# Kernel optimization log

Measured on AMD Instinct MI355X. Metric: run time of the kernel, lower is better.

## Reference

```python
import jax, jax.numpy as jnp
import numpy as np

N_NODES = 100000
N_EDGES = 3200000
IN_DIM = 128
HID = 128
K = 20  # n_gaussians


def gcn_conv(x, src, dst, W, b, n_nodes):
    """PyG GCNConv: add self-loops, symmetric normalization, linear transform.
    out = D^{-1/2} (A + I) D^{-1/2} (x @ W) + b, where D is degree of A+I.
    """
    h = x @ W  # [N, out_dim]
    # degree on A + I (self-loop contributes 1 to every node)
    deg = jax.ops.segment_sum(jnp.ones_like(dst, dtype=h.dtype), dst,
                              num_segments=n_nodes) + 1.0
    dis = jax.lax.rsqrt(deg)  # deg >= 1, safe
    norm = dis[src] * dis[dst]  # [E]
    # gather -> scale -> scatter-add (edges), plus self-loop term dis_i^2 * h_i
    agg = jax.ops.segment_sum(h[src] * norm[:, None], dst,
                              num_segments=n_nodes)
    agg = agg + h * (dis * dis)[:, None]
    return agg + b


def setup_inputs() -> dict:
    key = jax.random.key(0)
    ks = jax.random.split(key, 12)
    x = jax.random.normal(ks[0], (N_NODES, IN_DIM), dtype=jnp.float32)
    edge_index = jax.random.randint(ks[1], (2, N_EDGES), 0, N_NODES, dtype=jnp.int32)
    s = 1.0 / np.sqrt(HID)
    W1 = jax.random.uniform(ks[2], (IN_DIM, HID), jnp.float32, -s, s)
    b1 = jnp.zeros((HID,), jnp.float32)
    W2 = jax.random.uniform(ks[3], (HID, HID), jnp.float32, -s, s)
    b2 = jnp.zeros((HID,), jnp.float32)
    pi_W = jax.random.uniform(ks[4], (HID, K), jnp.float32, -s, s)
    pi_b = jnp.zeros((K,), jnp.float32)
    mu_W = jax.random.uniform(ks[5], (HID, K), jnp.float32, -s, s)
    mu_b = jnp.zeros((K,), jnp.float32)
    ls_W = jax.random.uniform(ks[6], (HID, K), jnp.float32, -s, s)
    ls_b = jnp.zeros((K,), jnp.float32)
    return {"x": x, "edge_index": edge_index, "W1": W1, "b1": b1,
            "W2": W2, "b2": b2, "pi_W": pi_W, "pi_b": pi_b,
            "mu_W": mu_W, "mu_b": mu_b, "ls_W": ls_W, "ls_b": ls_b}


def reference(x, edge_index, W1, b1, W2, b2, pi_W, pi_b, mu_W, mu_b, ls_W, ls_b):
    src, dst = edge_index[0], edge_index[1]
    n = x.shape[0]
    h = jax.nn.relu(gcn_conv(x, src, dst, W1, b1, n))
    h = jax.nn.relu(gcn_conv(h, src, dst, W2, b2, n))
    pi = jax.nn.softmax(h @ pi_W + pi_b, axis=1)
    mu = h @ mu_W + mu_b
    log_sigma = h @ ls_W + ls_b
    return (pi, mu, log_sigma)
```

## Files before the change

kernel.cpp:

```cpp
#include <hip/hip_runtime.h>
#include <hip/hip_fp16.h>
#include <cstdint>
#include <cstddef>

#define IN_DIM 128
#define HID    128
#define NG     20
#define T      4096
#define MAXB   400

typedef _Float16 half8 __attribute__((ext_vector_type(8)));
typedef _Float16 half4 __attribute__((ext_vector_type(4)));
typedef float    f32x4 __attribute__((ext_vector_type(4)));

__global__ void zero_ints(int* __restrict__ a, int n) {
  int i = blockIdx.x * blockDim.x + threadIdx.x;
  if (i < n) a[i] = 0;
}

__global__ __launch_bounds__(512) void binsort1(const int* __restrict__ src,
    const int* __restrict__ dst, int* __restrict__ tmp, int* __restrict__ bofs,
    int* __restrict__ bintot, int NBC, int E) {
  __shared__ int lhist[MAXB];
  __shared__ int lscan[512];
  __shared__ int lcur[MAXB];
  __shared__ int sbuf[T];
  int tid = threadIdx.x;
  int tile0 = blockIdx.x * T;
  int m = E - tile0; if (m > T) m = T;

  for (int i = tid; i < NBC; i += 512) lhist[i] = 0;
  __syncthreads();

  int dreg[8];
#pragma unroll
  for (int j = 0; j < 8; ++j) {
    int idx = j * 512 + tid;
    dreg[j] = -1;
    if (idx < m) {
      int d = dst[tile0 + idx];
      dreg[j] = d;
      atomicAdd(&lhist[d >> 8], 1);
    }
  }
  __syncthreads();

  int v = (tid < NBC) ? lhist[tid] : 0;
  lscan[tid] = v;
  __syncthreads();
  for (int o = 1; o < 512; o <<= 1) {
    int t = (tid >= o) ? lscan[tid - o] : 0;
    __syncthreads();
    lscan[tid] += t;
    __syncthreads();
  }
  if (tid < NBC) lcur[tid] = lscan[tid] - v;
  __syncthreads();

  int ST = NBC + 1;
  for (int i = tid; i < NBC; i += 512) bofs[(size_t)blockIdx.x * ST + i] = lcur[i];
  if (tid == 0) bofs[(size_t)blockIdx.x * ST + NBC] = m;
  for (int i = tid; i < NBC; i += 512)
    if (lhist[i]) atomicAdd(&bintot[i], lhist[i]);
  __syncthreads();

#pragma unroll
  for (int j = 0; j < 8; ++j) {
    int idx = j * 512 + tid;
    if (idx < m) {
      int d = dreg[j];
      int s = src[tile0 + idx];
      int slot = atomicAdd(&lcur[d >> 8], 1);
      sbuf[slot] = ((d & 255) << 17) | s;
    }
  }
  __syncthreads();

  int nv = m >> 2;
  int4* out4 = (int4*)(tmp + tile0);
  const int4* sb4 = (const int4*)sbuf;
  for (int i = tid; i < nv; i += 512) out4[i] = sb4[i];
  for (int i = (nv << 2) + tid; i < m; i += 512) tmp[tile0 + i] = sbuf[i];
}

__global__ __launch_bounds__(512) void binscan(const int* __restrict__ bintot,
                                               int* __restrict__ binbase, int NBC) {
  __shared__ int s[512];
  int tid = threadIdx.x;
  int v = (tid < NBC) ? bintot[tid] : 0;
  s[tid] = v;
  __syncthreads();
  for (int o = 1; o < 512; o <<= 1) {
    int t = (tid >= o) ? s[tid - o] : 0;
    __syncthreads();
    s[tid] += t;
    __syncthreads();
  }
  if (tid < NBC) binbase[tid] = s[tid] - v;
}

__global__ __launch_bounds__(1024) void binsort2(const int* __restrict__ tmp,
    const int* __restrict__ bofs, const int* __restrict__ binbase,
    int* __restrict__ csrc, int* __restrict__ cnt, float* __restrict__ dis,
    int* __restrict__ offs, int NBC, int nblk, int N) {
  __shared__ int lcnt[256];
  __shared__ int lsc[256];
  __shared__ int lcur2[256];
  int b = blockIdx.x;
  int tid = threadIdx.x;
  if (tid < 256) lcnt[tid] = 0;
  __syncthreads();
  int ST = NBC + 1;
  for (int r = tid; r < nblk; r += 1024) {
    int s = bofs[(size_t)r * ST + b];
    int e2 = bofs[(size_t)r * ST + b + 1];
    int base = r * T;
    for (int k = s; k < e2; ++k)
      atomicAdd(&lcnt[tmp[base + k] >> 17], 1);
  }
  __syncthreads();
  if (tid < 256) lsc[tid] = lcnt[tid];
  __syncthreads();
  for (int o = 1; o < 256; o <<= 1) {
    int t = 0;
    if (tid < 256 && tid >= o) t = lsc[tid - o];
    __syncthreads();
    if (tid < 256) lsc[tid] += t;
    __syncthreads();
  }
  int gbase = binbase[b];
  if (tid < 256) {
    int excl = lsc[tid] - lcnt[tid];
    lcur2[tid] = gbase + excl;
    int node = (b << 8) + tid;
    if (node < N) {
      cnt[node] = lcnt[tid];
      dis[node] = rsqrtf((float)lcnt[tid] + 1.0f);
      offs[node] = gbase + excl;
    }
  }
  __syncthreads();
  for (int r = tid; r < nblk; r += 1024) {
    int s = bofs[(size_t)r * ST + b];
    int e2 = bofs[(size_t)r * ST + b + 1];
    int base = r * T;
    for (int k = s; k < e2; ++k) {
      int rec = tmp[base + k];
      int pos = atomicAdd(&lcur2[rec >> 17], 1);
      csrc[pos] = rec & 0x1FFFF;
    }
  }
}

__global__ __launch_bounds__(256) void gemm128_mfma(const float* __restrict__ A,
                                                    const float* __restrict__ B,
                                                    __half* __restrict__ C, int M) {
  __shared__ _Float16 sA[128][136];
  const int tid = threadIdx.x;
  const int m0 = blockIdx.x * 128;

#pragma unroll
  for (int q = 0; q < 16; ++q) {
    int idx = q * 256 + tid;
    int r = idx >> 5;
    int cc = (idx & 31) << 2;
    float4 v = make_float4(0.f, 0.f, 0.f, 0.f);
    if (m0 + r < M) v = *(const float4*)(A + (size_t)(m0 + r) * 128 + cc);
    half4 hv;
    hv[0] = (_Float16)v.x; hv[1] = (_Float16)v.y;
    hv[2] = (_Float16)v.z; hv[3] = (_Float16)v.w;
    *(half4*)(&sA[r][cc]) = hv;
  }
  __syncthreads();

  const int wave = tid >> 6, lane = tid & 63;
  const int nbase = wave << 5;
  const int lrow = lane & 15;
  const int khi  = lane >> 4;

  half8 bf[2][4];
#pragma unroll
  for (int nf = 0; nf < 2; ++nf) {
    const float* wcol = B + (nbase + nf * 16 + lrow);
#pragma unroll
    for (int ks = 0; ks < 4; ++ks) {
      half8 hb;
#pragma unroll
      for (int rr = 0; rr < 8; ++rr)
        hb[rr] = (_Float16)wcol[(size_t)(ks * 32 + khi * 8 + rr) * 128];
      bf[nf][ks] = hb;
    }
  }

  f32x4 acc[8][2];
#pragma unroll
  for (int mf = 0; mf < 8; ++mf)
#pragma unroll
    for (int nf = 0; nf < 2; ++nf) acc[mf][nf] = (f32x4){0.f, 0.f, 0.f, 0.f};

#pragma unroll
  for (int mf = 0; mf < 8; ++mf) {
    const _Float16* ar = &sA[mf * 16 + lrow][khi * 8];
    half8 a0 = *(const half8*)(ar);
    half8 a1 = *(const half8*)(ar + 32);
    half8 a2 = *(const half8*)(ar + 64);
    half8 a3 = *(const half8*)(ar + 96);
    acc[mf][0] = __builtin_amdgcn_mfma_f32_16x16x32_f16(a0, bf[0][0], acc[mf][0], 0, 0, 0);
    acc[mf][1] = __builtin_amdgcn_mfma_f32_16x16x32_f16(a0, bf[1][0], acc[mf][1], 0, 0, 0);
    acc[mf][0] = __builtin_amdgcn_mfma_f32_16x16x32_f16(a1, bf[0][1], acc[mf][0], 0, 0, 0);
    acc[mf][1] = __builtin_amdgcn_mfma_f32_16x16x32_f16(a1, bf[1][1], acc[mf][1], 0, 0, 0);
    acc[mf][0] = __builtin_amdgcn_mfma_f32_16x16x32_f16(a2, bf[0][2], acc[mf][0], 0, 0, 0);
    acc[mf][1] = __builtin_amdgcn_mfma_f32_16x16x32_f16(a2, bf[1][2], acc[mf][1], 0, 0, 0);
    acc[mf][0] = __builtin_amdgcn_mfma_f32_16x16x32_f16(a3, bf[0][3], acc[mf][0], 0, 0, 0);
    acc[mf][1] = __builtin_amdgcn_mfma_f32_16x16x32_f16(a3, bf[1][3], acc[mf][1], 0, 0, 0);
  }

#pragma unroll
  for (int mf = 0; mf < 8; ++mf) {
    int r0 = mf * 16 + khi * 4;
#pragma unroll
    for (int nf = 0; nf < 2; ++nf) {
      int ccol = nbase + nf * 16 + lrow;
#pragma unroll
      for (int reg = 0; reg < 4; ++reg) {
        int r = m0 + r0 + reg;
        if (r < M) C[(size_t)r * 128 + ccol] = __float2half(acc[mf][nf][reg]);
      }
    }
  }
}

__global__ __launch_bounds__(256) void agg_kernel(const __half* __restrict__ h,
    const int* __restrict__ csrc,
    const int* __restrict__ offs, const int* __restrict__ cnt,
    const float* __restrict__ dis, const float* __restrict__ bias,
    float* __restrict__ out, int n) {
  int wave = threadIdx.x >> 6;
  int lane = threadIdx.x & 63;
  int i0 = (blockIdx.x * 4 + wave) * 2;
  if (i0 >= n) return;
  int i1 = i0 + 1;
  bool has1 = i1 < n;
  int c = lane * 2;

  int st0 = offs[i0];
  int m0  = cnt[i0];
  float d0 = dis[i0];
  int st1 = 0, m1 = 0;
  float d1 = 0.f;
  if (has1) { st1 = offs[i1]; m1 = cnt[i1]; d1 = dis[i1]; }

  float ax0 = 0.f, ay0 = 0.f, ax1 = 0.f, ay1 = 0.f;
  int mMax = m0 > m1 ? m0 : m1;

  for (int base = 0; base < mMax; base += 64) {
    int mcA = m0 - base; mcA = mcA < 0 ? 0 : (mcA > 64 ? 64 : mcA);
    int mcB = m1 - base; mcB = mcB < 0 ? 0 : (mcB > 64 ? 64 : mcB);
    int mc = mcA > mcB ? mcA : mcB;

    int sA = 0, sB = 0;
    float wA = 0.f, wB = 0.f;
    if (lane < mcA) sA = csrc[st0 + base + lane];
    if (lane < mcB) sB = csrc[st1 + base + lane];
    if (lane < mcA) wA = dis[sA] * d0;
    if (lane < mcB) wB = dis[sB] * d1;

    int j = 0;
    for (; j + 4 <= mc; j += 4) {
      int   a0 = __shfl(sA, j);
      int   a1 = __shfl(sA, j + 1);
      int   a2 = __shfl(sA, j + 2);
      int   a3 = __shfl(sA, j + 3);
      int   b0 = __shfl(sB, j);
      int   b1 = __shfl(sB, j + 1);
      int   b2 = __shfl(sB, j + 2);
      int   b3 = __shfl(sB, j + 3);
      float u0 = __shfl(wA, j);
      float u1 = __shfl(wA, j + 1);
      float u2 = __shfl(wA, j + 2);
      float u3 = __shfl(wA, j + 3);
      float v0 = __shfl(wB, j);
      float v1 = __shfl(wB, j + 1);
      float v2 = __shfl(wB, j + 2);
      float v3 = __shfl(wB, j + 3);
      float2 hA0 = __half22float2(*(const __half2*)(h + ((size_t)a0 << 7) + c));
      float2 hA1 = __half22float2(*(const __half2*)(h + ((size_t)a1 << 7) + c));
      float2 hA2 = __half22float2(*(const __half2*)(h + ((size_t)a2 << 7) + c));
      float2 hA3 = __half22float2(*(const __half2*)(h + ((size_t)a3 << 7) + c));
      float2 hB0 = __half22float2(*(const __half2*)(h + ((size_t)b0 << 7) + c));
      float2 hB1 = __half22float2(*(const __half2*)(h + ((size_t)b1 << 7) + c));
      float2 hB2 = __half22float2(*(const __half2*)(h + ((size_t)b2 << 7) + c));
      float2 hB3 = __half22float2(*(const __half2*)(h + ((size_t)b3 << 7) + c));
      ax0 = fmaf(hA0.x, u0, ax0); ay0 = fmaf(hA0.y, u0, ay0);
      ax0 = fmaf(hA1.x, u1, ax0); ay0 = fmaf(hA1.y, u1, ay0);
      ax0 = fmaf(hA2.x, u2, ax0); ay0 = fmaf(hA2.y, u2, ay0);
      ax0 = fmaf(hA3.x, u3, ax0); ay0 = fmaf(hA3.y, u3, ay0);
      ax1 = fmaf(hB0.x, v0, ax1); ay1 = fmaf(hB0.y, v0, ay1);
      ax1 = fmaf(hB1.x, v1, ax1); ay1 = fmaf(hB1.y, v1, ay1);
      ax1 = fmaf(hB2.x, v2, ax1); ay1 = fmaf(hB2.y, v2, ay1);
      ax1 = fmaf(hB3.x, v3, ax1); ay1 = fmaf(hB3.y, v3, ay1);
    }
    for (; j < mc; ++j) {
      int   a0 = __shfl(sA, j);
      int   b0 = __shfl(sB, j);
      float u0 = __shfl(wA, j);
      float v0 = __shfl(wB, j);
      float2 hA0 = __half22float2(*(const __half2*)(h + ((size_t)a0 << 7) + c));
      float2 hB0 = __half22float2(*(const __half2*)(h + ((size_t)b0 << 7) + c));
      ax0 = fmaf(hA0.x, u0, ax0); ay0 = fmaf(hA0.y, u0, ay0);
      ax1 = fmaf(hB0.x, v0, ax1); ay1 = fmaf(hB0.y, v0, ay1);
    }
  }

  float2 bv = *(const float2*)(bias + c);
  {
    float dd = d0 * d0;
    float2 hs = __half22float2(*(const __half2*)(h + ((size_t)i0 << 7) + c));
    float vx = fmaf(hs.x, dd, ax0) + bv.x;
    float vy = fmaf(hs.y, dd, ay0) + bv.y;
    *(float2*)(out + (size_t)i0 * 128 + c) = make_float2(fmaxf(vx, 0.f), fmaxf(vy, 0.f));
  }
  if (has1) {
    float dd = d1 * d1;
    float2 hs = __half22float2(*(const __half2*)(h + ((size_t)i1 << 7) + c));
    float vx = fmaf(hs.x, dd, ax1) + bv.x;
    float vy = fmaf(hs.y, dd, ay1) + bv.y;
    *(float2*)(out + (size_t)i1 * 128 + c) = make_float2(fmaxf(vx, 0.f), fmaxf(vy, 0.f));
  }
}

__global__ void pack_heads_w(const float* __restrict__ piW, const float* __restrict__ muW,
                             const float* __restrict__ lsW, float* __restrict__ W64) {
  int i = blockIdx.x * 256 + threadIdx.x;
  if (i >= 128 * 64) return;
  int k = i >> 6, j = i & 63;
  float v = 0.f;
  if (j < 20)      v = piW[k * 20 + j];
  else if (j < 40) v = muW[k * 20 + (j - 20)];
  else if (j < 60) v = lsW[k * 20 + (j - 40)];
  W64[i] = v;
}

#define KC 64
__global__ __launch_bounds__(256) void gemm_heads(const float* __restrict__ A,
                                                  const float* __restrict__ B,
                                                  float* __restrict__ C, int M) {
  __shared__ float sA[64][KC + 4];
  __shared__ float sB[KC][68];
  int tid = threadIdx.x;
  int m0 = blockIdx.x * 64;
  int tr = tid >> 4;
  int tc = tid & 15;
  float acc[4][4];
#pragma unroll
  for (int i = 0; i < 4; ++i)
#pragma unroll
    for (int j = 0; j < 4; ++j) acc[i][j] = 0.f;

  for (int k0 = 0; k0 < 128; k0 += KC) {
#pragma unroll
    for (int q = 0; q < 4; ++q) {
      int idx = q * 256 + tid;
      int r = idx >> 4;
      int kk = (idx & 15) << 2;
      float4 v = make_float4(0.f, 0.f, 0.f, 0.f);
      if (m0 + r < M) v = *(const float4*)(A + (size_t)(m0 + r) * 128 + k0 + kk);
      *(float4*)(&sA[r][kk]) = v;
    }
#pragma unroll
    for (int q = 0; q < 4; ++q) {
      int idx = q * 256 + tid;
      int kk = idx >> 4;
      int nn = (idx & 15) << 2;
      *(float4*)(&sB[kk][nn]) = *(const float4*)(B + (size_t)(k0 + kk) * 64 + nn);
    }
    __syncthreads();
#pragma unroll 4
    for (int k = 0; k < KC; k += 4) {
      float4 a0 = *(const float4*)(&sA[tr][k]);
      float4 a1 = *(const float4*)(&sA[tr + 16][k]);
      float4 a2 = *(const float4*)(&sA[tr + 32][k]);
      float4 a3 = *(const float4*)(&sA[tr + 48][k]);
#pragma unroll
      for (int u = 0; u < 4; ++u) {
        float4 b = *(const float4*)(&sB[k + u][tc * 4]);
        float av[4] = {((const float*)&a0)[u], ((const float*)&a1)[u],
                       ((const float*)&a2)[u], ((const float*)&a3)[u]};
#pragma unroll
        for (int i = 0; i < 4; ++i) {
          acc[i][0] = fmaf(av[i], b.x, acc[i][0]);
          acc[i][1] = fmaf(av[i], b.y, acc[i][1]);
          acc[i][2] = fmaf(av[i], b.z, acc[i][2]);
          acc[i][3] = fmaf(av[i], b.w, acc[i][3]);
        }
      }
    }
    __syncthreads();
  }
#pragma unroll
  for (int i = 0; i < 4; ++i) {
    int r = m0 + tr + 16 * i;
    if (r < M)
      *(float4*)(C + (size_t)r * 64 + tc * 4) =
          make_float4(acc[i][0], acc[i][1], acc[i][2], acc[i][3]);
  }
}

__global__ __launch_bounds__(256) void heads_post(const float* __restrict__ out60,
    const float* __restrict__ pib, const float* __restrict__ mub,
    const float* __restrict__ lsb, float* __restrict__ out, int n) {
  int wave = threadIdx.x >> 6, lane = threadIdx.x & 63;
  int node = blockIdx.x * 4 + wave;
  if (node >= n) return;
  float v = 0.f;
  if (lane < 60) {
    v = out60[(size_t)node * 64 + lane];
    v += (lane < 20) ? pib[lane] : (lane < 40) ? mub[lane - 20] : lsb[lane - 40];
  }
  float pv = (lane < 20) ? v : -__builtin_inff();
  float mx = pv;
  for (int o = 16; o > 0; o >>= 1) mx = fmaxf(mx, __shfl_down(mx, o, 32));
  mx = __shfl(mx, 0, 32);
  float ev = (lane < 20) ? expf(v - mx) : 0.f;
  float sm = ev;
  for (int o = 16; o > 0; o >>= 1) sm += __shfl_down(sm, o, 32);
  sm = __shfl(sm, 0, 32);

  size_t base = (size_t)n * NG;
  if (lane < 20)      out[(size_t)node * NG + lane] = ev / sm;
  else if (lane < 40) out[base + (size_t)node * NG + (lane - 20)] = v;
  else if (lane < 60) out[2 * base + (size_t)node * NG + (lane - 40)] = v;
}

extern "C" void kernel_launch(void* const* d_in, const int* in_sizes, int n_in,
                              void* d_out, int out_size, void* d_ws, size_t ws_size,
                              hipStream_t stream) {
  const float* x   = (const float*)d_in[0];
  const int*   ei  = (const int*)d_in[1];
  const float* W1  = (const float*)d_in[2];
  const float* b1  = (const float*)d_in[3];
  const float* W2  = (const float*)d_in[4];
  const float* b2  = (const float*)d_in[5];
  const float* piW = (const float*)d_in[6];
  const float* pib = (const float*)d_in[7];
  const float* muW = (const float*)d_in[8];
  const float* mub = (const float*)d_in[9];
  const float* lsW = (const float*)d_in[10];
  const float* lsb = (const float*)d_in[11];
  float* out = (float*)d_out;

  const int N = in_sizes[0] / IN_DIM;
  const int E = in_sizes[1] / 2;
  const int* src = ei;
  const int* dst = ei + E;

  const int NBC  = (N + 255) >> 8;
  const int nblk = (E + T - 1) / T;
  const int ST   = NBC + 1;

  char* p = (char*)d_ws;
  char* regionH = p;                        p += (size_t)N * HID * sizeof(__half);
  __half* h16  = (__half*)regionH;
  float* out60 = (float*)regionH;
  char* regionR = p;
  size_t szR = (size_t)N * HID * sizeof(float);
  size_t szT = (size_t)E * sizeof(int);
  p += (szR > szT ? szR : szT);
  int*   tmp    = (int*)regionR;
  float* bufB   = (float*)regionR;
  int*   csrc   = (int*)p;                  p += (size_t)E * sizeof(int);
  int*   bofs   = (int*)p;                  p += (size_t)nblk * ST * sizeof(int);
  int*   bintot = (int*)p;                  p += (size_t)MAXB * sizeof(int);
  int*   binbase= (int*)p;                  p += (size_t)MAXB * sizeof(int);
  int*   cnt    = (int*)p;                  p += (size_t)N * sizeof(int);
  int*   offs   = (int*)p;                  p += (size_t)N * sizeof(int);
  float* dis    = (float*)p;                p += (size_t)N * sizeof(float);
  float* W64    = (float*)p;                p += (size_t)128 * 64 * sizeof(float);

  zero_ints<<<(NBC + 255) / 256, 256, 0, stream>>>(bintot, NBC);
  binsort1<<<nblk, 512, 0, stream>>>(src, dst, tmp, bofs, bintot, NBC, E);
  binscan<<<1, 512, 0, stream>>>(bintot, binbase, NBC);
  binsort2<<<NBC, 1024, 0, stream>>>(tmp, bofs, binbase, csrc, cnt, dis, offs,
                                     NBC, nblk, N);
  pack_heads_w<<<(128 * 64 + 255) / 256, 256, 0, stream>>>(piW, muW, lsW, W64);

  const int NB8 = (N + 7) / 8;
  const int NBG = (N + 127) / 128;

  gemm128_mfma<<<NBG, 256, 0, stream>>>(x, W1, h16, N);
  agg_kernel<<<NB8, 256, 0, stream>>>(h16, csrc, offs, cnt, dis, b1, bufB, N);
  gemm128_mfma<<<NBG, 256, 0, stream>>>(bufB, W2, h16, N);
  agg_kernel<<<NB8, 256, 0, stream>>>(h16, csrc, offs, cnt, dis, b2, bufB, N);

  gemm_heads<<<(N + 63) / 64, 256, 0, stream>>>(bufB, W64, out60, N);
  heads_post<<<(N + 3) / 4, 256, 0, stream>>>(out60, pib, mub, lsb, out, N);
}
```

Measured before the change: 550.3 us.

## Store layer-1 activations in fp16, fuse head GEMM with softmax, pipeline weight loads

The first aggregation now writes its ReLU output in fp16, and the second GEMM reads it directly as fp16. This halves that intermediate's write and read traffic and drops a conversion. The head GEMM and its softmax/bias post-processing are merged into one kernel that stages results in shared memory, removing the out60 round trip and one launch. The MFMA GEMM also loads and converts weights per k-slice in a software-pipelined way instead of all upfront, which lowers register pressure but adds more shared memory in the head kernel.

```diff
diff --git a/kernel.cpp b/kernel.cpp
--- a/kernel.cpp
+++ b/kernel.cpp
@@ -152,68 +152,87 @@
   }
 }
 
-__global__ __launch_bounds__(256) void gemm128_mfma(const float* __restrict__ A,
+template<bool F16IN>
+__global__ __launch_bounds__(256) void gemm128_mfma(const void* __restrict__ Av,
                                                     const float* __restrict__ B,
                                                     __half* __restrict__ C, int M) {
   __shared__ _Float16 sA[128][136];
   const int tid = threadIdx.x;
   const int m0 = blockIdx.x * 128;
-
-#pragma unroll
-  for (int q = 0; q < 16; ++q) {
-    int idx = q * 256 + tid;
-    int r = idx >> 5;
-    int cc = (idx & 31) << 2;
-    float4 v = make_float4(0.f, 0.f, 0.f, 0.f);
-    if (m0 + r < M) v = *(const float4*)(A + (size_t)(m0 + r) * 128 + cc);
-    half4 hv;
-    hv[0] = (_Float16)v.x; hv[1] = (_Float16)v.y;
-    hv[2] = (_Float16)v.z; hv[3] = (_Float16)v.w;
-    *(half4*)(&sA[r][cc]) = hv;
-  }
-  __syncthreads();
-
   const int wave = tid >> 6, lane = tid & 63;
   const int nbase = wave << 5;
   const int lrow = lane & 15;
   const int khi  = lane >> 4;
-
-  half8 bf[2][4];
-#pragma unroll
-  for (int nf = 0; nf < 2; ++nf) {
-    const float* wcol = B + (nbase + nf * 16 + lrow);
-#pragma unroll
-    for (int ks = 0; ks < 4; ++ks) {
-      half8 hb;
+  const float* wcol = B + nbase + lrow;
+
+  float bA[2][8], bB[2][8];
+#pragma unroll
+  for (int nf = 0; nf < 2; ++nf)
+#pragma unroll
+    for (int rr = 0; rr < 8; ++rr)
+      bA[nf][rr] = wcol[(size_t)(khi * 8 + rr) * 128 + nf * 16];
+
+  if constexpr (F16IN) {
+    const __half* A = (const __half*)Av;
+#pragma unroll
+    for (int q = 0; q < 8; ++q) {
+      int idx = q * 256 + tid;
+      int r = idx >> 4;
+      int cc = (idx & 15) << 3;
+      half8 hv = {};
+      if (m0 + r < M) hv = *(const half8*)(A + (size_t)(m0 + r) * 128 + cc);
+      *(half8*)(&sA[r][cc]) = hv;
+    }
+  } else {
+    const float* A = (const float*)Av;
+#pragma unroll
+    for (int q = 0; q < 16; ++q) {
+      int idx = q * 256 + tid;
+      int r = idx >> 5;
+      int cc = (idx & 31) << 2;
+      float4 v = make_float4(0.f, 0.f, 0.f, 0.f);
+      if (m0 + r < M) v = *(const float4*)(A + (size_t)(m0 + r) * 128 + cc);
+      half4 hv;
+      hv[0] = (_Float16)v.x; hv[1] = (_Float16)v.y;
+      hv[2] = (_Float16)v.z; hv[3] = (_Float16)v.w;
+      *(half4*)(&sA[r][cc]) = hv;
+    }
+  }
+  __syncthreads();
+
+  f32x4 acc[8][2];
+#pragma unroll
+  for (int mf = 0; mf < 8; ++mf)
+#pragma unroll
+    for (int nf = 0; nf < 2; ++nf) acc[mf][nf] = (f32x4){0.f, 0.f, 0.f, 0.f};
+
+  auto loadB = [&](float (&dst)[2][8], int ks) {
+#pragma unroll
+    for (int nf = 0; nf < 2; ++nf)
 #pragma unroll
       for (int rr = 0; rr < 8; ++rr)
-        hb[rr] = (_Float16)wcol[(size_t)(ks * 32 + khi * 8 + rr) * 128];
-      bf[nf][ks] = hb;
-    }
-  }
-
-  f32x4 acc[8][2];
-#pragma unroll
-  for (int mf = 0; mf < 8; ++mf)
-#pragma unroll
-    for (int nf = 0; nf < 2; ++nf) acc[mf][nf] = (f32x4){0.f, 0.f, 0.f, 0.f};
-
-#pragma unroll
-  for (int mf = 0; mf < 8; ++mf) {
-    const _Float16* ar = &sA[mf * 16 + lrow][khi * 8];
-    half8 a0 = *(const half8*)(ar);
-    half8 a1 = *(const half8*)(ar + 32);
-    half8 a2 = *(const half8*)(ar + 64);
-    half8 a3 = *(const half8*)(ar + 96);
-    acc[mf][0] = __builtin_amdgcn_mfma_f32_16x16x32_f16(a0, bf[0][0], acc[mf][0], 0, 0, 0);
-    acc[mf][1] = __builtin_amdgcn_mfma_f32_16x16x32_f16(a0, bf[1][0], acc[mf][1], 0, 0, 0);
-    acc[mf][0] = __builtin_amdgcn_mfma_f32_16x16x32_f16(a1, bf[0][1], acc[mf][0], 0, 0, 0);
-    acc[mf][1] = __builtin_amdgcn_mfma_f32_16x16x32_f16(a1, bf[1][1], acc[mf][1], 0, 0, 0);
-    acc[mf][0] = __builtin_amdgcn_mfma_f32_16x16x32_f16(a2, bf[0][2], acc[mf][0], 0, 0, 0);
-    acc[mf][1] = __builtin_amdgcn_mfma_f32_16x16x32_f16(a2, bf[1][2], acc[mf][1], 0, 0, 0);
-    acc[mf][0] = __builtin_amdgcn_mfma_f32_16x16x32_f16(a3, bf[0][3], acc[mf][0], 0, 0, 0);
-    acc[mf][1] = __builtin_amdgcn_mfma_f32_16x16x32_f16(a3, bf[1][3], acc[mf][1], 0, 0, 0);
-  }
+        dst[nf][rr] = wcol[(size_t)(ks * 32 + khi * 8 + rr) * 128 + nf * 16];
+  };
+  half8 bf0, bf1;
+  auto cvtB = [&](float (&s)[2][8]) {
+#pragma unroll
+    for (int rr = 0; rr < 8; ++rr) {
+      bf0[rr] = (_Float16)s[0][rr];
+      bf1[rr] = (_Float16)s[1][rr];
+    }
+  };
+  auto mfmas = [&](int ks) {
+#pragma unroll
+    for (int mf = 0; mf < 8; ++mf) {
+      half8 a = *(const half8*)(&sA[mf * 16 + lrow][khi * 8 + ks * 32]);
+      acc[mf][0] = __builtin_amdgcn_mfma_f32_16x16x32_f16(a, bf0, acc[mf][0], 0, 0, 0);
+      acc[mf][1] = __builtin_amdgcn_mfma_f32_16x16x32_f16(a, bf1, acc[mf][1], 0, 0, 0);
+    }
+  };
+  cvtB(bA); loadB(bB, 1); mfmas(0);
+  cvtB(bB); loadB(bA, 2); mfmas(1);
+  cvtB(bA); loadB(bB, 3); mfmas(2);
+  cvtB(bB);               mfmas(3);
 
 #pragma unroll
   for (int mf = 0; mf < 8; ++mf) {
@@ -230,11 +249,12 @@
   }
 }
 
+template<typename OutT>
 __global__ __launch_bounds__(256) void agg_kernel(const __half* __restrict__ h,
     const int* __restrict__ csrc,
     const int* __restrict__ offs, const int* __restrict__ cnt,
     const float* __restrict__ dis, const float* __restrict__ bias,
-    float* __restrict__ out, int n) {
+    OutT* __restrict__ out, int n) {
   int wave = threadIdx.x >> 6;
   int lane = threadIdx.x & 63;
   int i0 = (blockIdx.x * 4 + wave) * 2;
@@ -316,16 +336,24 @@
   {
     float dd = d0 * d0;
     float2 hs = __half22float2(*(const __half2*)(h + ((size_t)i0 << 7) + c));
-    float vx = fmaf(hs.x, dd, ax0) + bv.x;
-    float vy = fmaf(hs.y, dd, ay0) + bv.y;
-    *(float2*)(out + (size_t)i0 * 128 + c) = make_float2(fmaxf(vx, 0.f), fmaxf(vy, 0.f));
+    float vx = fmaxf(fmaf(hs.x, dd, ax0) + bv.x, 0.f);
+    float vy = fmaxf(fmaf(hs.y, dd, ay0) + bv.y, 0.f);
+    if constexpr (sizeof(OutT) == 2) {
+      *(__half2*)((__half*)out + (size_t)i0 * 128 + c) = __floats2half2_rn(vx, vy);
+    } else {
+      *(float2*)((float*)out + (size_t)i0 * 128 + c) = make_float2(vx, vy);
+    }
   }
   if (has1) {
     float dd = d1 * d1;
     float2 hs = __half22float2(*(const __half2*)(h + ((size_t)i1 << 7) + c));
-    float vx = fmaf(hs.x, dd, ax1) + bv.x;
-    float vy = fmaf(hs.y, dd, ay1) + bv.y;
-    *(float2*)(out + (size_t)i1 * 128 + c) = make_float2(fmaxf(vx, 0.f), fmaxf(vy, 0.f));
+    float vx = fmaxf(fmaf(hs.x, dd, ax1) + bv.x, 0.f);
+    float vy = fmaxf(fmaf(hs.y, dd, ay1) + bv.y, 0.f);
+    if constexpr (sizeof(OutT) == 2) {
+      *(__half2*)((__half*)out + (size_t)i1 * 128 + c) = __floats2half2_rn(vx, vy);
+    } else {
+      *(float2*)((float*)out + (size_t)i1 * 128 + c) = make_float2(vx, vy);
+    }
   }
 }
 
@@ -342,11 +370,13 @@
 }
 
 #define KC 64
-__global__ __launch_bounds__(256) void gemm_heads(const float* __restrict__ A,
-                                                  const float* __restrict__ B,
-                                                  float* __restrict__ C, int M) {
+__global__ __launch_bounds__(256) void heads_fused(const float* __restrict__ A,
+    const float* __restrict__ B, const float* __restrict__ pib,
+    const float* __restrict__ mub, const float* __restrict__ lsb,
+    float* __restrict__ out, int n) {
   __shared__ float sA[64][KC + 4];
   __shared__ float sB[KC][68];
+  __shared__ float sOut[64][68];
   int tid = threadIdx.x;
   int m0 = blockIdx.x * 64;
   int tr = tid >> 4;
@@ -364,7 +394,7 @@
       int r = idx >> 4;
       int kk = (idx & 15) << 2;
       float4 v = make_float4(0.f, 0.f, 0.f, 0.f);
-      if (m0 + r < M) v = *(const float4*)(A + (size_t)(m0 + r) * 128 + k0 + kk);
+      if (m0 + r < n) v = *(const float4*)(A + (size_t)(m0 + r) * 128 + k0 + kk);
       *(float4*)(&sA[r][kk]) = v;
     }
 #pragma unroll
@@ -397,39 +427,36 @@
     }
     __syncthreads();
   }
-#pragma unroll
-  for (int i = 0; i < 4; ++i) {
-    int r = m0 + tr + 16 * i;
-    if (r < M)
-      *(float4*)(C + (size_t)r * 64 + tc * 4) =
-          make_float4(acc[i][0], acc[i][1], acc[i][2], acc[i][3]);
-  }
-}
-
-__global__ __launch_bounds__(256) void heads_post(const float* __restrict__ out60,
-    const float* __restrict__ pib, const float* __restrict__ mub,
-    const float* __restrict__ lsb, float* __restrict__ out, int n) {
-  int wave = threadIdx.x >> 6, lane = threadIdx.x & 63;
-  int node = blockIdx.x * 4 + wave;
-  if (node >= n) return;
-  float v = 0.f;
-  if (lane < 60) {
-    v = out60[(size_t)node * 64 + lane];
-    v += (lane < 20) ? pib[lane] : (lane < 40) ? mub[lane - 20] : lsb[lane - 40];
-  }
-  float pv = (lane < 20) ? v : -__builtin_inff();
-  float mx = pv;
-  for (int o = 16; o > 0; o >>= 1) mx = fmaxf(mx, __shfl_down(mx, o, 32));
-  mx = __shfl(mx, 0, 32);
-  float ev = (lane < 20) ? expf(v - mx) : 0.f;
-  float sm = ev;
-  for (int o = 16; o > 0; o >>= 1) sm += __shfl_down(sm, o, 32);
-  sm = __shfl(sm, 0, 32);
-
-  size_t base = (size_t)n * NG;
-  if (lane < 20)      out[(size_t)node * NG + lane] = ev / sm;
-  else if (lane < 40) out[base + (size_t)node * NG + (lane - 20)] = v;
-  else if (lane < 60) out[2 * base + (size_t)node * NG + (lane - 40)] = v;
+
+#pragma unroll
+  for (int i = 0; i < 4; ++i)
+#pragma unroll
+    for (int j = 0; j < 4; ++j) sOut[tr + 16 * i][tc * 4 + j] = acc[i][j];
+  __syncthreads();
+
+  int wave = tid >> 6, lane = tid & 63;
+  size_t nb = (size_t)n * NG;
+  for (int t = 0; t < 16; ++t) {
+    int rr = wave * 16 + t;
+    int node = m0 + rr;
+    if (node >= n) break;
+    float v = 0.f;
+    if (lane < 60) {
+      v = sOut[rr][lane];
+      v += (lane < 20) ? pib[lane] : (lane < 40) ? mub[lane - 20] : lsb[lane - 40];
+    }
+    float pv = (lane < 20) ? v : -__builtin_inff();
+    float mx = pv;
+    for (int o = 16; o > 0; o >>= 1) mx = fmaxf(mx, __shfl_down(mx, o, 32));
+    mx = __shfl(mx, 0, 32);
+    float ev = (lane < 20) ? expf(v - mx) : 0.f;
+    float sm = ev;
+    for (int o = 16; o > 0; o >>= 1) sm += __shfl_down(sm, o, 32);
+    sm = __shfl(sm, 0, 32);
+    if (lane < 20)      out[(size_t)node * NG + lane] = ev / sm;
+    else if (lane < 40) out[nb + (size_t)node * NG + (lane - 20)] = v;
+    else if (lane < 60) out[2 * nb + (size_t)node * NG + (lane - 40)] = v;
+  }
 }
 
 extern "C" void kernel_launch(void* const* d_in, const int* in_sizes, int n_in,
@@ -461,13 +488,13 @@
   char* p = (char*)d_ws;
   char* regionH = p;                        p += (size_t)N * HID * sizeof(__half);
   __half* h16  = (__half*)regionH;
-  float* out60 = (float*)regionH;
   char* regionR = p;
   size_t szR = (size_t)N * HID * sizeof(float);
   size_t szT = (size_t)E * sizeof(int);
   p += (szR > szT ? szR : szT);
-  int*   tmp    = (int*)regionR;
-  float* bufB   = (float*)regionR;
+  int*    tmp    = (int*)regionR;
+  __half* bufB16 = (__half*)regionR;
+  float*  bufB   = (float*)regionR;
   int*   csrc   = (int*)p;                  p += (size_t)E * sizeof(int);
   int*   bofs   = (int*)p;                  p += (size_t)nblk * ST * sizeof(int);
   int*   bintot = (int*)p;                  p += (size_t)MAXB * sizeof(int);
@@ -487,11 +514,12 @@
   const int NB8 = (N + 7) / 8;
   const int NBG = (N + 127) / 128;
 
-  gemm128_mfma<<<NBG, 256, 0, stream>>>(x, W1, h16, N);
-  agg_kernel<<<NB8, 256, 0, stream>>>(h16, csrc, offs, cnt, dis, b1, bufB, N);
-  gemm128_mfma<<<NBG, 256, 0, stream>>>(bufB, W2, h16, N);
-  agg_kernel<<<NB8, 256, 0, stream>>>(h16, csrc, offs, cnt, dis, b2, bufB, N);
-
-  gemm_heads<<<(N + 63) / 64, 256, 0, stream>>>(bufB, W64, out60, N);
-  heads_post<<<(N + 3) / 4, 256, 0, stream>>>(out60, pib, mub, lsb, out, N);
-}
+  gemm128_mfma<false><<<NBG, 256, 0, stream>>>(x, W1, h16, N);
+  agg_kernel<__half><<<NB8, 256, 0, stream>>>(h16, csrc, offs, cnt, dis, b1,
+                                              bufB16, N);
+  gemm128_mfma<true><<<NBG, 256, 0, stream>>>(bufB16, W2, h16, N);
+  agg_kernel<float><<<NB8, 256, 0, stream>>>(h16, csrc, offs, cnt, dis, b2,
+                                             bufB, N);
+
+  heads_fused<<<(N + 63) / 64, 256, 0, stream>>>(bufB, W64, pib, mub, lsb, out, N);
+}
```

New measurement: 547.3 us. About the same (-0.5%).
